# Kernel optimization log

Measured on AMD Instinct MI355X. Metric: run time of the kernel, lower is better.

## Reference

```python
import jax, jax.numpy as jnp
import numpy as np

EMBEDDING_DIM = 128
NEG = -1000.0


def setup_inputs() -> dict:
    key = jax.random.key(0)
    ks = jax.random.split(key, 7)
    B, S_src, S_tgt, D = 2, 4096, 512, EMBEDDING_DIM
    return {
        "input_embeddings": jax.random.normal(ks[0], (B, S_src, D), dtype=jnp.float32),
        "token_attention_masks_source": jax.random.randint(ks[1], (B, S_src), 0, 2, dtype=jnp.int32),
        "token_attention_masks_target": jax.random.randint(ks[2], (B, S_tgt), 0, 2, dtype=jnp.int32),
        "encoder_output_embedding": jax.random.normal(ks[3], (B, S_tgt, D), dtype=jnp.float32),
        "w_query": jax.random.uniform(ks[4], (D, D), dtype=jnp.float32),
        "w_key": jax.random.uniform(ks[5], (D, D), dtype=jnp.float32),
        "w_value": jax.random.uniform(ks[6], (D, D), dtype=jnp.float32),
    }


def reference(input_embeddings, token_attention_masks_source,
              token_attention_masks_target, encoder_output_embedding,
              w_query, w_key, w_value):
    # Encoder self-attention branch (attention_type='encoder'), num_heads=1.
    D = w_query.shape[0]
    q = jnp.einsum('bsd,de->bse', input_embeddings, w_query)   # [B,S,D]
    k = jnp.einsum('bsd,de->bse', input_embeddings, w_key)     # [B,S,D]
    v = jnp.einsum('bsd,de->bse', input_embeddings, w_value)   # [B,S,D]
    scores = jnp.einsum('bsd,btd->bst', q, k) / jnp.sqrt(jnp.float32(D))
    # Original adds mask along the QUERY axis: mask[B,S] -> unsqueeze(-1).
    add_mask = jnp.where(token_attention_masks_source == 0, NEG, 0.0).astype(scores.dtype)
    scores = scores + add_mask[:, :, None]
    probs = jax.nn.softmax(scores, axis=2)                      # softmax over keys
    out = jnp.einsum('bst,btd->bsd', probs, v)                  # [B,S,D]
    return out
```

## Files before the change

kernel.cpp:

```cpp
#include <hip/hip_runtime.h>
#include <hip/hip_bf16.h>

#define S_SRC 4096
#define DIM 128
#define BATCH 2
#define KSPLIT 8
#define NQG 512

typedef unsigned short u16;
typedef unsigned int u32;
typedef __bf16 bf16x8 __attribute__((ext_vector_type(8)));
typedef float f32x4 __attribute__((ext_vector_type(4)));
typedef u32 u32x4 __attribute__((ext_vector_type(4)));

__device__ __forceinline__ __bf16 bf_hi(float x) { return (__bf16)x; }
__device__ __forceinline__ __bf16 bf_lo(float x, __bf16 h) { return (__bf16)(x - (float)h); }
__device__ __forceinline__ u16 bfu(__bf16 h) { return __builtin_bit_cast(u16, h); }
__device__ __forceinline__ u16 f2bu(float x) { return __builtin_bit_cast(u16, (__bf16)x); }
__device__ __forceinline__ float bu2f(u16 u) { return (float)__builtin_bit_cast(__bf16, u); }
__device__ __forceinline__ u32 pk2(float lo, float hi) {
  return (u32)f2bu(lo) | ((u32)f2bu(hi) << 16);
}
__device__ __forceinline__ void g2l16(const u16* src, u16* ldst) {
  __builtin_amdgcn_global_load_lds((const __attribute__((address_space(1))) void*)src,
                                   (__attribute__((address_space(3))) void*)ldst, 16, 0, 0);
}

__global__ __launch_bounds__(256) void k_wsplit(const float* __restrict__ wq,
                                                const float* __restrict__ wk,
                                                const float* __restrict__ wv,
                                                u16* __restrict__ wt) {
  int idx = blockIdx.x * 256 + threadIdx.x;
  int mat = idx >> 14;
  int r = idx & 16383;
  int d = r >> 7, e = r & 127;
  const float* w = (mat == 0) ? wq : ((mat == 1) ? wk : wv);
  float x = w[r];
  if (mat == 0) x *= 0.08838834764831845f;
  __bf16 h = bf_hi(x);
  __bf16 l = bf_lo(x, h);
  wt[((mat * 2 + 0) * 128 + e) * 128 + d] = bfu(h);
  wt[((mat * 2 + 1) * 128 + e) * 128 + d] = bfu(l);
}

__global__ __launch_bounds__(256) void k_proj(const float* __restrict__ X,
                                              const u16* __restrict__ wt,
                                              u16* __restrict__ Qh, u16* __restrict__ Ql,
                                              u16* __restrict__ Kh, u16* __restrict__ Kl,
                                              u16* __restrict__ VT) {
  const int b = blockIdx.x >> 7;
  const int tile = blockIdx.x & 127;
  const int tid = threadIdx.x;
  const int w = tid >> 6, lane = tid & 63, g = lane >> 4, l16 = lane & 15;

  bf16x8 a_h[2][4], a_l[2][4];
#pragma unroll
  for (int mf = 0; mf < 2; ++mf) {
    int row = tile * 32 + mf * 16 + l16;
    const float* xr = X + ((size_t)b * S_SRC + row) * DIM;
#pragma unroll
    for (int kf = 0; kf < 4; ++kf) {
      int d0 = kf * 32 + g * 8;
      f32x4 x0 = *(const f32x4*)(xr + d0);
      f32x4 x1 = *(const f32x4*)(xr + d0 + 4);
#pragma unroll
      for (int j = 0; j < 4; ++j) {
        __bf16 h0 = bf_hi(x0[j]);
        __bf16 h1 = bf_hi(x1[j]);
        a_h[mf][kf][j] = h0;
        a_l[mf][kf][j] = bf_lo(x0[j], h0);
        a_h[mf][kf][4 + j] = h1;
        a_l[mf][kf][4 + j] = bf_lo(x1[j], h1);
      }
    }
  }

#pragma unroll
  for (int mat = 0; mat < 3; ++mat) {
    const u16* wth = wt + (mat * 2 + 0) * 16384;
    const u16* wtl = wt + (mat * 2 + 1) * 16384;
#pragma unroll
    for (int nf = 0; nf < 2; ++nf) {
      int col = w * 32 + nf * 16 + l16;
      f32x4 acc[2];
      acc[0] = (f32x4){0.f, 0.f, 0.f, 0.f};
      acc[1] = (f32x4){0.f, 0.f, 0.f, 0.f};
#pragma unroll
      for (int kf = 0; kf < 4; ++kf) {
        int d0 = kf * 32 + g * 8;
        bf16x8 bh = *(const bf16x8*)(const void*)(wth + col * 128 + d0);
        bf16x8 bl = *(const bf16x8*)(const void*)(wtl + col * 128 + d0);
#pragma unroll
        for (int mf = 0; mf < 2; ++mf) {
          acc[mf] = __builtin_amdgcn_mfma_f32_16x16x32_bf16(a_h[mf][kf], bh, acc[mf], 0, 0, 0);
          acc[mf] = __builtin_amdgcn_mfma_f32_16x16x32_bf16(a_h[mf][kf], bl, acc[mf], 0, 0, 0);
          acc[mf] = __builtin_amdgcn_mfma_f32_16x16x32_bf16(a_l[mf][kf], bh, acc[mf], 0, 0, 0);
        }
      }
#pragma unroll
      for (int mf = 0; mf < 2; ++mf)
#pragma unroll
        for (int r = 0; r < 4; ++r) {
          int row = tile * 32 + mf * 16 + g * 4 + r;
          float v = acc[mf][r];
          if (mat == 2) {
            VT[((size_t)b * DIM + col) * S_SRC + row] = f2bu(v);
          } else {
            __bf16 h = bf_hi(v);
            __bf16 l = bf_lo(v, h);
            size_t o = ((size_t)b * S_SRC + row) * DIM + col;
            if (mat == 0) { Qh[o] = bfu(h); Ql[o] = bfu(l); }
            else          { Kh[o] = bfu(h); Kl[o] = bfu(l); }
          }
        }
    }
  }
}

__global__ __launch_bounds__(512, 4) void k_attn(const u16* __restrict__ Qh, const u16* __restrict__ Ql,
                                                 const u16* __restrict__ Kh, const u16* __restrict__ Kl,
                                                 const u16* __restrict__ VT,
                                                 float* __restrict__ Pm, float* __restrict__ Pl,
                                                 u16* __restrict__ PO) {
  const int bid = blockIdx.x;
  const int lid = (bid & 7) * 64 + (bid >> 3);
  const int qb = lid & 63;
  const int sp = lid >> 6;
  const int b = qb >> 5;
  const int tid = threadIdx.x;
  const int w = tid >> 6, lane = tid & 63, g = lane >> 4, l16 = lane & 15;

  __shared__ alignas(16) u16 kbuf[2][8192];
  __shared__ alignas(16) u16 vbuf[2][4096];

  const int gr0 = qb * 128 + w * 16;
  bf16x8 q_h[4], q_l[4];
  {
    const u16* qph = Qh + ((size_t)gr0 + l16) * DIM;
    const u16* qpl = Ql + ((size_t)gr0 + l16) * DIM;
#pragma unroll
    for (int kf = 0; kf < 4; ++kf) {
      int d0 = kf * 32 + g * 8;
      q_h[kf] = *(const bf16x8*)(const void*)(qph + d0);
      q_l[kf] = *(const bf16x8*)(const void*)(qpl + d0);
    }
  }

  f32x4 acc[8];
#pragma unroll
  for (int nf = 0; nf < 8; ++nf) acc[nf] = (f32x4){0.f, 0.f, 0.f, 0.f};
  float m_run = -1e30f, l_run = 0.f;

  const int key_base = sp * (S_SRC / KSPLIT);
  const u16* KhB = Kh + (size_t)b * S_SRC * DIM;
  const u16* KlB = Kl + (size_t)b * S_SRC * DIM;
  const u16* VTB = VT + (size_t)b * DIM * S_SRC;

  const int kkey = tid >> 4, kcp = tid & 15;
  const int kcs = (kcp ^ (kkey & 15)) << 3;
  const int vd = tid >> 2, vcp = tid & 3;
  const int vcs = (vcp ^ ((vd >> 1) & 3)) << 3;
  const int wbase = w * 512;

#define STAGE(BUF, KEY0)                                                        \
  {                                                                             \
    const u16* sH = KhB + ((size_t)((KEY0) + kkey)) * DIM + kcs;                \
    const u16* sL = KlB + ((size_t)((KEY0) + kkey)) * DIM + kcs;                \
    const u16* sV = VTB + (size_t)vd * S_SRC + (KEY0) + vcs;                    \
    g2l16(sH, &kbuf[BUF][wbase]);                                               \
    g2l16(sL, &kbuf[BUF][4096 + wbase]);                                        \
    g2l16(sV, &vbuf[BUF][wbase]);                                               \
  }

  STAGE(0, key_base)

  const int mg = ((g & 1) << 1) | (g >> 1);
  int cur = 0;
  for (int i = 0; i < S_SRC / KSPLIT / 32; ++i) {
    if (i + 1 < S_SRC / KSPLIT / 32) {
      STAGE(cur ^ 1, key_base + (i + 1) * 32)
      asm volatile("s_waitcnt vmcnt(3)" ::: "memory");
    } else {
      asm volatile("s_waitcnt vmcnt(0)" ::: "memory");
    }
    __builtin_amdgcn_s_barrier();

    const u16* kb = kbuf[cur];
    f32x4 s0 = (f32x4){0.f, 0.f, 0.f, 0.f};
    f32x4 s1 = (f32x4){0.f, 0.f, 0.f, 0.f};
    __builtin_amdgcn_s_setprio(1);
#pragma unroll
    for (int kf = 0; kf < 4; ++kf) {
      int cs = ((kf * 4 + g) ^ l16) << 3;
      bf16x8 kh0 = *(const bf16x8*)(const void*)(kb + l16 * 128 + cs);
      bf16x8 kl0 = *(const bf16x8*)(const void*)(kb + 4096 + l16 * 128 + cs);
      bf16x8 kh1 = *(const bf16x8*)(const void*)(kb + (16 + l16) * 128 + cs);
      bf16x8 kl1 = *(const bf16x8*)(const void*)(kb + 4096 + (16 + l16) * 128 + cs);
      s0 = __builtin_amdgcn_mfma_f32_16x16x32_bf16(kh0, q_h[kf], s0, 0, 0, 0);
      s0 = __builtin_amdgcn_mfma_f32_16x16x32_bf16(kh0, q_l[kf], s0, 0, 0, 0);
      s0 = __builtin_amdgcn_mfma_f32_16x16x32_bf16(kl0, q_h[kf], s0, 0, 0, 0);
      s1 = __builtin_amdgcn_mfma_f32_16x16x32_bf16(kh1, q_h[kf], s1, 0, 0, 0);
      s1 = __builtin_amdgcn_mfma_f32_16x16x32_bf16(kh1, q_l[kf], s1, 0, 0, 0);
      s1 = __builtin_amdgcn_mfma_f32_16x16x32_bf16(kl1, q_h[kf], s1, 0, 0, 0);
    }
    __builtin_amdgcn_s_setprio(0);

    float mx = fmaxf(fmaxf(fmaxf(s0[0], s0[1]), fmaxf(s0[2], s0[3])),
                     fmaxf(fmaxf(s1[0], s1[1]), fmaxf(s1[2], s1[3])));
    mx = fmaxf(mx, __shfl_xor(mx, 16, 64));
    mx = fmaxf(mx, __shfl_xor(mx, 32, 64));
    if (!__all(mx - m_run <= 8.0f)) {
      float mn = fmaxf(m_run, mx);
      float f = __expf(m_run - mn);
      l_run *= f;
      m_run = mn;
      float fr0 = __shfl(f, g * 4 + 0, 64);
      float fr1 = __shfl(f, g * 4 + 1, 64);
      float fr2 = __shfl(f, g * 4 + 2, 64);
      float fr3 = __shfl(f, g * 4 + 3, 64);
#pragma unroll
      for (int nf = 0; nf < 8; ++nf) {
        acc[nf][0] *= fr0; acc[nf][1] *= fr1; acc[nf][2] *= fr2; acc[nf][3] *= fr3;
      }
    }
    float e0 = __expf(s0[0] - m_run), e1 = __expf(s0[1] - m_run);
    float e2 = __expf(s0[2] - m_run), e3 = __expf(s0[3] - m_run);
    float e4 = __expf(s1[0] - m_run), e5 = __expf(s1[1] - m_run);
    float e6 = __expf(s1[2] - m_run), e7 = __expf(s1[3] - m_run);
    float sm = ((e0 + e1) + (e2 + e3)) + ((e4 + e5) + (e6 + e7));
    sm += __shfl_xor(sm, 16, 64);
    sm += __shfl_xor(sm, 32, 64);
    l_run += sm;

    u32 w0 = pk2(e0, e1), w1 = pk2(e2, e3), w2 = pk2(e4, e5), w3 = pk2(e6, e7);
    u32 x0 = __shfl_xor(w0, 16, 64), x1 = __shfl_xor(w1, 16, 64);
    u32 x2 = __shfl_xor(w2, 16, 64), x3 = __shfl_xor(w3, 16, 64);
    bool odd = (g & 1);
    u32x4 pw;
    pw.x = odd ? x2 : w0;
    pw.y = odd ? x3 : w1;
    pw.z = odd ? w2 : x0;
    pw.w = odd ? w3 : x1;
    bf16x8 pa = __builtin_bit_cast(bf16x8, pw);

    const u16* vb = vbuf[cur];
    __builtin_amdgcn_s_setprio(1);
#pragma unroll
    for (int nf = 0; nf < 8; ++nf) {
      int d = nf * 16 + l16;
      bf16x8 vf = *(const bf16x8*)(const void*)(vb + d * 32 + ((mg ^ ((d >> 1) & 3)) << 3));
      acc[nf] = __builtin_amdgcn_mfma_f32_16x16x32_bf16(pa, vf, acc[nf], 0, 0, 0);
    }
    __builtin_amdgcn_s_setprio(0);

    __builtin_amdgcn_s_barrier();
    cur ^= 1;
  }

  const int pidx = sp * NQG + (gr0 >> 4);
  u16* po = PO + (size_t)pidx * 16 * DIM;
#pragma unroll
  for (int nf = 0; nf < 8; ++nf)
#pragma unroll
    for (int r = 0; r < 4; ++r)
      po[(g * 4 + r) * DIM + nf * 16 + l16] = f2bu(acc[nf][r]);
  if (lane < 16) {
    Pm[pidx * 16 + l16] = m_run;
    Pl[pidx * 16 + l16] = l_run;
  }
#undef STAGE
}

__global__ __launch_bounds__(64) void k_comb(const float* __restrict__ Pm,
                                             const float* __restrict__ Pl,
                                             const u16* __restrict__ PO,
                                             float* __restrict__ out) {
  const int qg = blockIdx.x;
  const int tid = threadIdx.x;

  __shared__ float sc[KSPLIT][16];
  if (tid < 16) {
    float m = -1e30f;
#pragma unroll
    for (int s = 0; s < KSPLIT; ++s) m = fmaxf(m, Pm[(s * NQG + qg) * 16 + tid]);
    float den = 0.f;
    float e[KSPLIT];
#pragma unroll
    for (int s = 0; s < KSPLIT; ++s) {
      e[s] = __expf(Pm[(s * NQG + qg) * 16 + tid] - m);
      den += Pl[(s * NQG + qg) * 16 + tid] * e[s];
    }
    float inv = 1.0f / den;
#pragma unroll
    for (int s = 0; s < KSPLIT; ++s) sc[s][tid] = e[s] * inv;
  }
  __syncthreads();

  float* op = out + (size_t)qg * 16 * DIM;
  for (int i = tid; i < 16 * DIM; i += 64) {
    int row = i >> 7;
    float acc = 0.f;
#pragma unroll
    for (int s = 0; s < KSPLIT; ++s)
      acc += bu2f(PO[(size_t)(s * NQG + qg) * 16 * DIM + i]) * sc[s][row];
    op[i] = acc;
  }
}

extern "C" void kernel_launch(void* const* d_in, const int* in_sizes, int n_in,
                              void* d_out, int out_size, void* d_ws, size_t ws_size,
                              hipStream_t stream) {
  const float* X  = (const float*)d_in[0];
  const float* wq = (const float*)d_in[4];
  const float* wk = (const float*)d_in[5];
  const float* wv = (const float*)d_in[6];
  float* out = (float*)d_out;

  u16* WT = (u16*)d_ws;
  u16* Qh = WT + 3 * 2 * 128 * 128;
  u16* Ql = Qh + (size_t)BATCH * S_SRC * DIM;
  u16* Kh = Ql + (size_t)BATCH * S_SRC * DIM;
  u16* Kl = Kh + (size_t)BATCH * S_SRC * DIM;
  u16* VT = Kl + (size_t)BATCH * S_SRC * DIM;
  float* Pm = (float*)(VT + (size_t)BATCH * S_SRC * DIM);
  float* Pl = Pm + (size_t)KSPLIT * NQG * 16;
  u16* PO = (u16*)(Pl + (size_t)KSPLIT * NQG * 16);

  hipLaunchKernelGGL(k_wsplit, dim3(192), dim3(256), 0, stream, wq, wk, wv, WT);
  hipLaunchKernelGGL(k_proj, dim3(BATCH * S_SRC / 32), dim3(256), 0, stream,
                     X, WT, Qh, Ql, Kh, Kl, VT);
  hipLaunchKernelGGL(k_attn, dim3(64 * KSPLIT), dim3(512), 0, stream,
                     Qh, Ql, Kh, Kl, VT, Pm, Pl, PO);
  hipLaunchKernelGGL(k_comb, dim3(NQG), dim3(64), 0, stream, Pm, Pl, PO, out);
}
```

Baseline: 73.55 us.

## Process two query groups per wave, raise KV split to 16, split projection by matrix

The attention kernel now uses 256-thread blocks where each wave handles 32 query rows (two 16-row groups). Each K/V tile loaded into LDS is reused for twice as many queries per wave, and the key dimension is split 16 ways instead of 8 when workspace allows. The projection kernel is also split across three times as many blocks, one per weight matrix, to expose more parallelism. The cost is higher register pressure from doubled accumulators, and more partial results for the combine kernel to read and merge.

```diff
diff --git a/kernel.cpp b/kernel.cpp
--- a/kernel.cpp
+++ b/kernel.cpp
@@ -4,7 +4,7 @@
 #define S_SRC 4096
 #define DIM 128
 #define BATCH 2
-#define KSPLIT 8
+#define NQB 64
 #define NQG 512
 
 typedef unsigned short u16;
@@ -25,6 +25,7 @@
   __builtin_amdgcn_global_load_lds((const __attribute__((address_space(1))) void*)src,
                                    (__attribute__((address_space(3))) void*)ldst, 16, 0, 0);
 }
+#define MFMA __builtin_amdgcn_mfma_f32_16x16x32_bf16
 
 __global__ __launch_bounds__(256) void k_wsplit(const float* __restrict__ wq,
                                                 const float* __restrict__ wk,
@@ -48,8 +49,10 @@
                                               u16* __restrict__ Qh, u16* __restrict__ Ql,
                                               u16* __restrict__ Kh, u16* __restrict__ Kl,
                                               u16* __restrict__ VT) {
-  const int b = blockIdx.x >> 7;
-  const int tile = blockIdx.x & 127;
+  const int mat = blockIdx.x >> 8;
+  const int t = blockIdx.x & 255;
+  const int b = t >> 7;
+  const int tile = t & 127;
   const int tid = threadIdx.x;
   const int w = tid >> 6, lane = tid & 63, g = lane >> 4, l16 = lane & 15;
 
@@ -75,57 +78,55 @@
     }
   }
 
-#pragma unroll
-  for (int mat = 0; mat < 3; ++mat) {
-    const u16* wth = wt + (mat * 2 + 0) * 16384;
-    const u16* wtl = wt + (mat * 2 + 1) * 16384;
-#pragma unroll
-    for (int nf = 0; nf < 2; ++nf) {
-      int col = w * 32 + nf * 16 + l16;
-      f32x4 acc[2];
-      acc[0] = (f32x4){0.f, 0.f, 0.f, 0.f};
-      acc[1] = (f32x4){0.f, 0.f, 0.f, 0.f};
-#pragma unroll
-      for (int kf = 0; kf < 4; ++kf) {
-        int d0 = kf * 32 + g * 8;
-        bf16x8 bh = *(const bf16x8*)(const void*)(wth + col * 128 + d0);
-        bf16x8 bl = *(const bf16x8*)(const void*)(wtl + col * 128 + d0);
-#pragma unroll
-        for (int mf = 0; mf < 2; ++mf) {
-          acc[mf] = __builtin_amdgcn_mfma_f32_16x16x32_bf16(a_h[mf][kf], bh, acc[mf], 0, 0, 0);
-          acc[mf] = __builtin_amdgcn_mfma_f32_16x16x32_bf16(a_h[mf][kf], bl, acc[mf], 0, 0, 0);
-          acc[mf] = __builtin_amdgcn_mfma_f32_16x16x32_bf16(a_l[mf][kf], bh, acc[mf], 0, 0, 0);
+  const u16* wth = wt + (mat * 2 + 0) * 16384;
+  const u16* wtl = wt + (mat * 2 + 1) * 16384;
+#pragma unroll
+  for (int nf = 0; nf < 2; ++nf) {
+    int col = w * 32 + nf * 16 + l16;
+    f32x4 acc[2];
+    acc[0] = (f32x4){0.f, 0.f, 0.f, 0.f};
+    acc[1] = (f32x4){0.f, 0.f, 0.f, 0.f};
+#pragma unroll
+    for (int kf = 0; kf < 4; ++kf) {
+      int d0 = kf * 32 + g * 8;
+      bf16x8 bh = *(const bf16x8*)(const void*)(wth + col * 128 + d0);
+      bf16x8 bl = *(const bf16x8*)(const void*)(wtl + col * 128 + d0);
+#pragma unroll
+      for (int mf = 0; mf < 2; ++mf) {
+        acc[mf] = MFMA(a_h[mf][kf], bh, acc[mf], 0, 0, 0);
+        acc[mf] = MFMA(a_h[mf][kf], bl, acc[mf], 0, 0, 0);
+        acc[mf] = MFMA(a_l[mf][kf], bh, acc[mf], 0, 0, 0);
+      }
+    }
+#pragma unroll
+    for (int mf = 0; mf < 2; ++mf)
+#pragma unroll
+      for (int r = 0; r < 4; ++r) {
+        int row = tile * 32 + mf * 16 + g * 4 + r;
+        float v = acc[mf][r];
+        if (mat == 2) {
+          VT[((size_t)b * DIM + col) * S_SRC + row] = f2bu(v);
+        } else {
+          __bf16 h = bf_hi(v);
+          __bf16 l = bf_lo(v, h);
+          size_t o = ((size_t)b * S_SRC + row) * DIM + col;
+          if (mat == 0) { Qh[o] = bfu(h); Ql[o] = bfu(l); }
+          else          { Kh[o] = bfu(h); Kl[o] = bfu(l); }
         }
       }
-#pragma unroll
-      for (int mf = 0; mf < 2; ++mf)
-#pragma unroll
-        for (int r = 0; r < 4; ++r) {
-          int row = tile * 32 + mf * 16 + g * 4 + r;
-          float v = acc[mf][r];
-          if (mat == 2) {
-            VT[((size_t)b * DIM + col) * S_SRC + row] = f2bu(v);
-          } else {
-            __bf16 h = bf_hi(v);
-            __bf16 l = bf_lo(v, h);
-            size_t o = ((size_t)b * S_SRC + row) * DIM + col;
-            if (mat == 0) { Qh[o] = bfu(h); Ql[o] = bfu(l); }
-            else          { Kh[o] = bfu(h); Kl[o] = bfu(l); }
-          }
-        }
-    }
-  }
-}
-
-__global__ __launch_bounds__(512, 4) void k_attn(const u16* __restrict__ Qh, const u16* __restrict__ Ql,
+  }
+}
+
+__global__ __launch_bounds__(256, 3) void k_attn(const u16* __restrict__ Qh, const u16* __restrict__ Ql,
                                                  const u16* __restrict__ Kh, const u16* __restrict__ Kl,
                                                  const u16* __restrict__ VT,
                                                  float* __restrict__ Pm, float* __restrict__ Pl,
-                                                 u16* __restrict__ PO) {
+                                                 u16* __restrict__ PO, int nsp) {
+  const int cpx = (NQB * nsp) >> 3;
   const int bid = blockIdx.x;
-  const int lid = (bid & 7) * 64 + (bid >> 3);
+  const int lid = (bid & 7) * cpx + (bid >> 3);
+  const int sp = lid >> 6;
   const int qb = lid & 63;
-  const int sp = lid >> 6;
   const int b = qb >> 5;
   const int tid = threadIdx.x;
   const int w = tid >> 6, lane = tid & 63, g = lane >> 4, l16 = lane & 15;
@@ -133,115 +134,146 @@
   __shared__ alignas(16) u16 kbuf[2][8192];
   __shared__ alignas(16) u16 vbuf[2][4096];
 
-  const int gr0 = qb * 128 + w * 16;
-  bf16x8 q_h[4], q_l[4];
-  {
-    const u16* qph = Qh + ((size_t)gr0 + l16) * DIM;
-    const u16* qpl = Ql + ((size_t)gr0 + l16) * DIM;
+  const int gr0 = qb * 128 + w * 32;
+  bf16x8 q_h[2][4], q_l[2][4];
+#pragma unroll
+  for (int qg = 0; qg < 2; ++qg) {
+    const u16* qph = Qh + ((size_t)gr0 + qg * 16 + l16) * DIM;
+    const u16* qpl = Ql + ((size_t)gr0 + qg * 16 + l16) * DIM;
 #pragma unroll
     for (int kf = 0; kf < 4; ++kf) {
       int d0 = kf * 32 + g * 8;
-      q_h[kf] = *(const bf16x8*)(const void*)(qph + d0);
-      q_l[kf] = *(const bf16x8*)(const void*)(qpl + d0);
-    }
-  }
-
-  f32x4 acc[8];
-#pragma unroll
-  for (int nf = 0; nf < 8; ++nf) acc[nf] = (f32x4){0.f, 0.f, 0.f, 0.f};
-  float m_run = -1e30f, l_run = 0.f;
-
-  const int key_base = sp * (S_SRC / KSPLIT);
+      q_h[qg][kf] = *(const bf16x8*)(const void*)(qph + d0);
+      q_l[qg][kf] = *(const bf16x8*)(const void*)(qpl + d0);
+    }
+  }
+
+  f32x4 acc[2][8];
+#pragma unroll
+  for (int qg = 0; qg < 2; ++qg)
+#pragma unroll
+    for (int nf = 0; nf < 8; ++nf) acc[qg][nf] = (f32x4){0.f, 0.f, 0.f, 0.f};
+  float m0 = -1e30f, m1 = -1e30f, l0 = 0.f, l1 = 0.f;
+
+  const int keys_per = S_SRC / nsp;
+  const int key_base = sp * keys_per;
+  const int niter = keys_per >> 5;
+
   const u16* KhB = Kh + (size_t)b * S_SRC * DIM;
   const u16* KlB = Kl + (size_t)b * S_SRC * DIM;
   const u16* VTB = VT + (size_t)b * DIM * S_SRC;
 
   const int kkey = tid >> 4, kcp = tid & 15;
-  const int kcs = (kcp ^ (kkey & 15)) << 3;
+  const int kco = (kcp ^ (kkey & 15)) << 3;
   const int vd = tid >> 2, vcp = tid & 3;
-  const int vcs = (vcp ^ ((vd >> 1) & 3)) << 3;
-  const int wbase = w * 512;
-
-#define STAGE(BUF, KEY0)                                                        \
-  {                                                                             \
-    const u16* sH = KhB + ((size_t)((KEY0) + kkey)) * DIM + kcs;                \
-    const u16* sL = KlB + ((size_t)((KEY0) + kkey)) * DIM + kcs;                \
-    const u16* sV = VTB + (size_t)vd * S_SRC + (KEY0) + vcs;                    \
-    g2l16(sH, &kbuf[BUF][wbase]);                                               \
-    g2l16(sL, &kbuf[BUF][4096 + wbase]);                                        \
-    g2l16(sV, &vbuf[BUF][wbase]);                                               \
+  const int vco = (vcp ^ ((vd >> 1) & 3)) << 3;
+  const int wb = w * 512;
+
+#define STAGE(BUF, KEY0)                                                          \
+  {                                                                               \
+    g2l16(KhB + ((size_t)((KEY0) + kkey)) * DIM + kco,      &kbuf[BUF][wb]);      \
+    g2l16(KhB + ((size_t)((KEY0) + 16 + kkey)) * DIM + kco, &kbuf[BUF][2048 + wb]); \
+    g2l16(KlB + ((size_t)((KEY0) + kkey)) * DIM + kco,      &kbuf[BUF][4096 + wb]); \
+    g2l16(KlB + ((size_t)((KEY0) + 16 + kkey)) * DIM + kco, &kbuf[BUF][6144 + wb]); \
+    g2l16(VTB + (size_t)vd * S_SRC + (KEY0) + vco,          &vbuf[BUF][wb]);      \
+    g2l16(VTB + (size_t)(64 + vd) * S_SRC + (KEY0) + vco,   &vbuf[BUF][2048 + wb]); \
   }
 
   STAGE(0, key_base)
 
   const int mg = ((g & 1) << 1) | (g >> 1);
   int cur = 0;
-  for (int i = 0; i < S_SRC / KSPLIT / 32; ++i) {
-    if (i + 1 < S_SRC / KSPLIT / 32) {
+  for (int i = 0; i < niter; ++i) {
+    if (i + 1 < niter) {
       STAGE(cur ^ 1, key_base + (i + 1) * 32)
-      asm volatile("s_waitcnt vmcnt(3)" ::: "memory");
+      asm volatile("s_waitcnt vmcnt(6)" ::: "memory");
     } else {
       asm volatile("s_waitcnt vmcnt(0)" ::: "memory");
     }
     __builtin_amdgcn_s_barrier();
 
     const u16* kb = kbuf[cur];
-    f32x4 s0 = (f32x4){0.f, 0.f, 0.f, 0.f};
-    f32x4 s1 = (f32x4){0.f, 0.f, 0.f, 0.f};
+    f32x4 s00, s01, s10, s11;
+    s00 = s01 = s10 = s11 = (f32x4){0.f, 0.f, 0.f, 0.f};
     __builtin_amdgcn_s_setprio(1);
 #pragma unroll
     for (int kf = 0; kf < 4; ++kf) {
       int cs = ((kf * 4 + g) ^ l16) << 3;
       bf16x8 kh0 = *(const bf16x8*)(const void*)(kb + l16 * 128 + cs);
       bf16x8 kl0 = *(const bf16x8*)(const void*)(kb + 4096 + l16 * 128 + cs);
+      s00 = MFMA(kh0, q_h[0][kf], s00, 0, 0, 0);
+      s00 = MFMA(kh0, q_l[0][kf], s00, 0, 0, 0);
+      s00 = MFMA(kl0, q_h[0][kf], s00, 0, 0, 0);
+      s10 = MFMA(kh0, q_h[1][kf], s10, 0, 0, 0);
+      s10 = MFMA(kh0, q_l[1][kf], s10, 0, 0, 0);
+      s10 = MFMA(kl0, q_h[1][kf], s10, 0, 0, 0);
       bf16x8 kh1 = *(const bf16x8*)(const void*)(kb + (16 + l16) * 128 + cs);
       bf16x8 kl1 = *(const bf16x8*)(const void*)(kb + 4096 + (16 + l16) * 128 + cs);
-      s0 = __builtin_amdgcn_mfma_f32_16x16x32_bf16(kh0, q_h[kf], s0, 0, 0, 0);
-      s0 = __builtin_amdgcn_mfma_f32_16x16x32_bf16(kh0, q_l[kf], s0, 0, 0, 0);
-      s0 = __builtin_amdgcn_mfma_f32_16x16x32_bf16(kl0, q_h[kf], s0, 0, 0, 0);
-      s1 = __builtin_amdgcn_mfma_f32_16x16x32_bf16(kh1, q_h[kf], s1, 0, 0, 0);
-      s1 = __builtin_amdgcn_mfma_f32_16x16x32_bf16(kh1, q_l[kf], s1, 0, 0, 0);
-      s1 = __builtin_amdgcn_mfma_f32_16x16x32_bf16(kl1, q_h[kf], s1, 0, 0, 0);
+      s01 = MFMA(kh1, q_h[0][kf], s01, 0, 0, 0);
+      s01 = MFMA(kh1, q_l[0][kf], s01, 0, 0, 0);
+      s01 = MFMA(kl1, q_h[0][kf], s01, 0, 0, 0);
+      s11 = MFMA(kh1, q_h[1][kf], s11, 0, 0, 0);
+      s11 = MFMA(kh1, q_l[1][kf], s11, 0, 0, 0);
+      s11 = MFMA(kl1, q_h[1][kf], s11, 0, 0, 0);
     }
     __builtin_amdgcn_s_setprio(0);
 
-    float mx = fmaxf(fmaxf(fmaxf(s0[0], s0[1]), fmaxf(s0[2], s0[3])),
-                     fmaxf(fmaxf(s1[0], s1[1]), fmaxf(s1[2], s1[3])));
-    mx = fmaxf(mx, __shfl_xor(mx, 16, 64));
-    mx = fmaxf(mx, __shfl_xor(mx, 32, 64));
-    if (!__all(mx - m_run <= 8.0f)) {
-      float mn = fmaxf(m_run, mx);
-      float f = __expf(m_run - mn);
-      l_run *= f;
-      m_run = mn;
-      float fr0 = __shfl(f, g * 4 + 0, 64);
-      float fr1 = __shfl(f, g * 4 + 1, 64);
-      float fr2 = __shfl(f, g * 4 + 2, 64);
-      float fr3 = __shfl(f, g * 4 + 3, 64);
-#pragma unroll
-      for (int nf = 0; nf < 8; ++nf) {
-        acc[nf][0] *= fr0; acc[nf][1] *= fr1; acc[nf][2] *= fr2; acc[nf][3] *= fr3;
+    bf16x8 pa0, pa1;
+#pragma unroll
+    for (int qg = 0; qg < 2; ++qg) {
+      f32x4 sA = qg ? s10 : s00;
+      f32x4 sB = qg ? s11 : s01;
+      float mr = qg ? m1 : m0;
+      float lr = qg ? l1 : l0;
+      float mx = fmaxf(fmaxf(fmaxf(sA[0], sA[1]), fmaxf(sA[2], sA[3])),
+                       fmaxf(fmaxf(sB[0], sB[1]), fmaxf(sB[2], sB[3])));
+      mx = fmaxf(mx, __shfl_xor(mx, 16, 64));
+      mx = fmaxf(mx, __shfl_xor(mx, 32, 64));
+      if (!__all(mx - mr <= 8.0f)) {
+        float mn = fmaxf(mr, mx);
+        float f = __expf(mr - mn);
+        lr *= f;
+        mr = mn;
+        float fr0 = __shfl(f, g * 4 + 0, 64);
+        float fr1 = __shfl(f, g * 4 + 1, 64);
+        float fr2 = __shfl(f, g * 4 + 2, 64);
+        float fr3 = __shfl(f, g * 4 + 3, 64);
+        if (qg == 0) {
+#pragma unroll
+          for (int nf = 0; nf < 8; ++nf) {
+            acc[0][nf][0] *= fr0; acc[0][nf][1] *= fr1;
+            acc[0][nf][2] *= fr2; acc[0][nf][3] *= fr3;
+          }
+        } else {
+#pragma unroll
+          for (int nf = 0; nf < 8; ++nf) {
+            acc[1][nf][0] *= fr0; acc[1][nf][1] *= fr1;
+            acc[1][nf][2] *= fr2; acc[1][nf][3] *= fr3;
+          }
+        }
       }
-    }
-    float e0 = __expf(s0[0] - m_run), e1 = __expf(s0[1] - m_run);
-    float e2 = __expf(s0[2] - m_run), e3 = __expf(s0[3] - m_run);
-    float e4 = __expf(s1[0] - m_run), e5 = __expf(s1[1] - m_run);
-    float e6 = __expf(s1[2] - m_run), e7 = __expf(s1[3] - m_run);
-    float sm = ((e0 + e1) + (e2 + e3)) + ((e4 + e5) + (e6 + e7));
-    sm += __shfl_xor(sm, 16, 64);
-    sm += __shfl_xor(sm, 32, 64);
-    l_run += sm;
-
-    u32 w0 = pk2(e0, e1), w1 = pk2(e2, e3), w2 = pk2(e4, e5), w3 = pk2(e6, e7);
-    u32 x0 = __shfl_xor(w0, 16, 64), x1 = __shfl_xor(w1, 16, 64);
-    u32 x2 = __shfl_xor(w2, 16, 64), x3 = __shfl_xor(w3, 16, 64);
-    bool odd = (g & 1);
-    u32x4 pw;
-    pw.x = odd ? x2 : w0;
-    pw.y = odd ? x3 : w1;
-    pw.z = odd ? w2 : x0;
-    pw.w = odd ? w3 : x1;
-    bf16x8 pa = __builtin_bit_cast(bf16x8, pw);
+      float e0 = __expf(sA[0] - mr), e1 = __expf(sA[1] - mr);
+      float e2 = __expf(sA[2] - mr), e3 = __expf(sA[3] - mr);
+      float e4 = __expf(sB[0] - mr), e5 = __expf(sB[1] - mr);
+      float e6 = __expf(sB[2] - mr), e7 = __expf(sB[3] - mr);
+      float sm = ((e0 + e1) + (e2 + e3)) + ((e4 + e5) + (e6 + e7));
+      sm += __shfl_xor(sm, 16, 64);
+      sm += __shfl_xor(sm, 32, 64);
+      lr += sm;
+      if (qg == 0) { m0 = mr; l0 = lr; } else { m1 = mr; l1 = lr; }
+
+      u32 w0 = pk2(e0, e1), w1 = pk2(e2, e3), w2 = pk2(e4, e5), w3 = pk2(e6, e7);
+      u32 x0 = __shfl_xor(w0, 16, 64), x1 = __shfl_xor(w1, 16, 64);
+      u32 x2 = __shfl_xor(w2, 16, 64), x3 = __shfl_xor(w3, 16, 64);
+      bool odd = (g & 1);
+      u32x4 pw;
+      pw.x = odd ? x2 : w0;
+      pw.y = odd ? x3 : w1;
+      pw.z = odd ? w2 : x0;
+      pw.w = odd ? w3 : x1;
+      if (qg == 0) pa0 = __builtin_bit_cast(bf16x8, pw);
+      else         pa1 = __builtin_bit_cast(bf16x8, pw);
+    }
 
     const u16* vb = vbuf[cur];
     __builtin_amdgcn_s_setprio(1);
@@ -249,7 +281,8 @@
     for (int nf = 0; nf < 8; ++nf) {
       int d = nf * 16 + l16;
       bf16x8 vf = *(const bf16x8*)(const void*)(vb + d * 32 + ((mg ^ ((d >> 1) & 3)) << 3));
-      acc[nf] = __builtin_amdgcn_mfma_f32_16x16x32_bf16(pa, vf, acc[nf], 0, 0, 0);
+      acc[0][nf] = MFMA(pa0, vf, acc[0][nf], 0, 0, 0);
+      acc[1][nf] = MFMA(pa1, vf, acc[1][nf], 0, 0, 0);
     }
     __builtin_amdgcn_s_setprio(0);
 
@@ -257,53 +290,50 @@
     cur ^= 1;
   }
 
-  const int pidx = sp * NQG + (gr0 >> 4);
-  u16* po = PO + (size_t)pidx * 16 * DIM;
-#pragma unroll
-  for (int nf = 0; nf < 8; ++nf)
-#pragma unroll
-    for (int r = 0; r < 4; ++r)
-      po[(g * 4 + r) * DIM + nf * 16 + l16] = f2bu(acc[nf][r]);
-  if (lane < 16) {
-    Pm[pidx * 16 + l16] = m_run;
-    Pl[pidx * 16 + l16] = l_run;
-  }
+  const int pidx0 = sp * NQG + (gr0 >> 4);
+#pragma unroll
+  for (int qg = 0; qg < 2; ++qg) {
+    u16* po = PO + (size_t)(pidx0 + qg) * 16 * DIM;
+#pragma unroll
+    for (int nf = 0; nf < 8; ++nf)
+#pragma unroll
+      for (int r = 0; r < 4; ++r)
+        po[(g * 4 + r) * DIM + nf * 16 + l16] = f2bu(acc[qg][nf][r]);
+  }
+  if (g == 0) { Pm[pidx0 * 16 + l16] = m0; Pl[pidx0 * 16 + l16] = l0; }
+  if (g == 1) { Pm[(pidx0 + 1) * 16 + l16] = m1; Pl[(pidx0 + 1) * 16 + l16] = l1; }
 #undef STAGE
 }
 
 __global__ __launch_bounds__(64) void k_comb(const float* __restrict__ Pm,
                                              const float* __restrict__ Pl,
                                              const u16* __restrict__ PO,
-                                             float* __restrict__ out) {
+                                             float* __restrict__ out, int nsp) {
   const int qg = blockIdx.x;
   const int tid = threadIdx.x;
 
-  __shared__ float sc[KSPLIT][16];
+  __shared__ float sc[16][16];
   if (tid < 16) {
     float m = -1e30f;
-#pragma unroll
-    for (int s = 0; s < KSPLIT; ++s) m = fmaxf(m, Pm[(s * NQG + qg) * 16 + tid]);
+    for (int s = 0; s < nsp; ++s) m = fmaxf(m, Pm[(s * NQG + qg) * 16 + tid]);
     float den = 0.f;
-    float e[KSPLIT];
-#pragma unroll
-    for (int s = 0; s < KSPLIT; ++s) {
-      e[s] = __expf(Pm[(s * NQG + qg) * 16 + tid] - m);
-      den += Pl[(s * NQG + qg) * 16 + tid] * e[s];
+    for (int s = 0; s < nsp; ++s) {
+      float e = __expf(Pm[(s * NQG + qg) * 16 + tid] - m);
+      sc[s][tid] = e;
+      den += Pl[(s * NQG + qg) * 16 + tid] * e;
     }
     float inv = 1.0f / den;
-#pragma unroll
-    for (int s = 0; s < KSPLIT; ++s) sc[s][tid] = e[s] * inv;
+    for (int s = 0; s < nsp; ++s) sc[s][tid] *= inv;
   }
   __syncthreads();
 
   float* op = out + (size_t)qg * 16 * DIM;
   for (int i = tid; i < 16 * DIM; i += 64) {
     int row = i >> 7;
-    float acc = 0.f;
-#pragma unroll
-    for (int s = 0; s < KSPLIT; ++s)
-      acc += bu2f(PO[(size_t)(s * NQG + qg) * 16 * DIM + i]) * sc[s][row];
-    op[i] = acc;
+    float a = 0.f;
+    for (int s = 0; s < nsp; ++s)
+      a += bu2f(PO[(size_t)(s * NQG + qg) * 16 * DIM + i]) * sc[s][row];
+    op[i] = a;
   }
 }
 
@@ -322,14 +352,20 @@
   u16* Kh = Ql + (size_t)BATCH * S_SRC * DIM;
   u16* Kl = Kh + (size_t)BATCH * S_SRC * DIM;
   u16* VT = Kl + (size_t)BATCH * S_SRC * DIM;
+
+  size_t fixed_b = (size_t)(3 * 2 * 128 * 128) * 2 + (size_t)5 * BATCH * S_SRC * DIM * 2;
+  int nsp = 16;
+  size_t need = fixed_b + (size_t)nsp * NQG * 16 * 8 + (size_t)nsp * NQG * 16 * DIM * 2;
+  if (ws_size < need) nsp = 8;
+
   float* Pm = (float*)(VT + (size_t)BATCH * S_SRC * DIM);
-  float* Pl = Pm + (size_t)KSPLIT * NQG * 16;
-  u16* PO = (u16*)(Pl + (size_t)KSPLIT * NQG * 16);
+  float* Pl = Pm + (size_t)nsp * NQG * 16;
+  u16* PO = (u16*)(Pl + (size_t)nsp * NQG * 16);
 
   hipLaunchKernelGGL(k_wsplit, dim3(192), dim3(256), 0, stream, wq, wk, wv, WT);
-  hipLaunchKernelGGL(k_proj, dim3(BATCH * S_SRC / 32), dim3(256), 0, stream,
+  hipLaunchKernelGGL(k_proj, dim3(3 * 256), dim3(256), 0, stream,
                      X, WT, Qh, Ql, Kh, Kl, VT);
-  hipLaunchKernelGGL(k_attn, dim3(64 * KSPLIT), dim3(512), 0, stream,
-                     Qh, Ql, Kh, Kl, VT, Pm, Pl, PO);
-  hipLaunchKernelGGL(k_comb, dim3(NQG), dim3(64), 0, stream, Pm, Pl, PO, out);
-}
+  hipLaunchKernelGGL(k_attn, dim3(NQB * nsp), dim3(256), 0, stream,
+                     Qh, Ql, Kh, Kl, VT, Pm, Pl, PO, nsp);
+  hipLaunchKernelGGL(k_comb, dim3(NQG), dim3(64), 0, stream, Pm, Pl, PO, out, nsp);
+}
```

Measured after the change: 125.3 us. +70.3%, slower.
